# Kernel tuning notes

Hardware: AMD Instinct MI355X
Metric: run time of the kernel (lower is better)

Reference implementation:

```python
import jax, jax.numpy as jnp
import numpy as np

N_NODES = 20000
N_EDGES = 640000
D = 128            # node feature dim
NUM_HEADS = 4      # = num_irreps of edge_sh (lmax=3, 0e+1o+2e+3o)
HEAD_DIM = D // NUM_HEADS
IR_DIMS = np.array([1, 3, 5, 7])  # dims of each irrep; sum = 16
AVG_NUM_NEIGHBORS = 32.0


def setup_inputs() -> dict:
    key = jax.random.key(0)
    ks = jax.random.split(key, 20)
    inp = {
        "edge_sh": jax.random.normal(ks[0], (N_EDGES, int(IR_DIMS.sum())), jnp.float32),
        "node_feats": jax.random.normal(ks[1], (N_NODES, D), jnp.float32),
        "edge_feats": jax.random.normal(ks[2], (N_EDGES, 64), jnp.float32),
        "chi_scalar": jax.random.normal(ks[3], (N_EDGES, 64), jnp.float32),
        "cutoffs": jax.random.uniform(ks[4], (N_EDGES,), jnp.float32),
        "senders": jax.random.randint(ks[5], (N_EDGES,), 0, N_NODES),
        "receivers": jax.random.randint(ks[6], (N_EDGES,), 0, N_NODES),
        # radial MLP: 64 -> 128 -> 128 (silu between)
        "W_rad1": jax.random.normal(ks[7], (64, 128), jnp.float32) / np.sqrt(64),
        "b_rad1": jnp.zeros((128,), jnp.float32),
        "W_rad2": jax.random.normal(ks[8], (128, 128), jnp.float32) / np.sqrt(128),
        "b_rad2": jnp.zeros((128,), jnp.float32),
        # spherical-scalar MLP: 64 -> 128 -> 128
        "W_sph1": jax.random.normal(ks[9], (64, 128), jnp.float32) / np.sqrt(64),
        "b_sph1": jnp.zeros((128,), jnp.float32),
        "W_sph2": jax.random.normal(ks[10], (128, 128), jnp.float32) / np.sqrt(128),
        "b_sph2": jnp.zeros((128,), jnp.float32),
        # Q/K projections, no bias
        "Wq": jax.random.normal(ks[11], (D, D), jnp.float32) / np.sqrt(D),
        "Wk": jax.random.normal(ks[12], (D, D), jnp.float32) / np.sqrt(D),
    }
    return inp


def reference(edge_sh, node_feats, edge_feats, chi_scalar, cutoffs, senders,
              receivers, W_rad1, b_rad1, W_rad2, b_rad2, W_sph1, b_sph1,
              W_sph2, b_sph2, Wq, Wk):
    silu = jax.nn.silu
    # edge filter: radial MLP + spherical-scalar MLP
    w = silu(edge_feats @ W_rad1 + b_rad1) @ W_rad2 + b_rad2      # [E, D]
    w = w + (silu(chi_scalar @ W_sph1 + b_sph1) @ W_sph2 + b_sph2)
    w = w.reshape(-1, NUM_HEADS, HEAD_DIM)                        # [E, H, hd]
    # gathered queries/keys
    q = (node_feats @ Wq).reshape(-1, NUM_HEADS, HEAD_DIM)[receivers]
    k = (node_feats @ Wk).reshape(-1, NUM_HEADS, HEAD_DIM)[senders]
    # filter-scaled attention: per-edge, per-head scalar
    alpha = (q * w * k).sum(axis=-1) * (1.0 / np.sqrt(HEAD_DIM))  # [E, H]
    alpha = alpha * cutoffs[:, None]
    # aligned_mul: broadcast per-irrep weight over each irrep's dim (mul=1)
    y = jnp.repeat(alpha, IR_DIMS, axis=-1)                       # [E, 16]
    msg = edge_sh * y
    # scatter_sum into receivers
    chi = jax.ops.segment_sum(msg, receivers, num_segments=N_NODES)
    return chi / AVG_NUM_NEIGHBORS
```

## Files before the change

### kernel.cpp

```cpp
#include <hip/hip_runtime.h>
#include <cmath>

#define NNODES 20000
#define NEDGES 640000
#define DDIM   128
#define TN     16
#define BE     64

typedef __attribute__((ext_vector_type(8))) short bf16x8;
typedef __attribute__((ext_vector_type(4))) float f32x4;
typedef __attribute__((ext_vector_type(4))) unsigned short us4;

__device__ __forceinline__ unsigned short f2bf(float x) {
    union { float f; unsigned u; } v; v.f = x;
    unsigned r = v.u + 0x7FFFu + ((v.u >> 16) & 1u);
    return (unsigned short)(r >> 16);
}
__device__ __forceinline__ float bf2f(unsigned short h) {
    union { unsigned u; float f; } v; v.u = ((unsigned)h) << 16; return v.f;
}
__device__ __forceinline__ unsigned cvtpk(float lo, float hi) {
    unsigned r;
    asm("v_cvt_pk_bf16_f32 %0, %1, %2" : "=v"(r) : "v"(lo), "v"(hi));
    return r;
}

__global__ void pack_weights(const float* __restrict__ W, unsigned short* __restrict__ dst)
{
    const int f  = blockIdx.x;
    const int kt = f >> 3, nt = f & 7;
    const int t  = threadIdx.x;
#pragma unroll
    for (int ii = 0; ii < 2; ii++) {
        const int idx  = t * 2 + ii;
        const int lane = idx >> 3, i = idx & 7;
        const int k = kt * 32 + (lane >> 4) * 8 + i;
        const int n = nt * 16 + (lane & 15);
        dst[f * 512 + idx] = f2bf(W[k * 128 + n]);
    }
}

__global__ __launch_bounds__(256) void qk_proj_kernel(
    const float* __restrict__ nf, const float* __restrict__ Wq,
    const float* __restrict__ Wk, unsigned short* __restrict__ qbuf,
    unsigned short* __restrict__ kbuf)
{
    __shared__ float s_nf[TN * DDIM];
    const int t  = threadIdx.x;
    const int n0 = blockIdx.x * TN;
    {
        const float4* src = (const float4*)(nf + (size_t)n0 * DDIM);
        float4* dst = (float4*)s_nf;
        for (int i = t; i < TN * DDIM / 4; i += 256) dst[i] = src[i];
    }
    __syncthreads();

    const int j = t & 127;
    const float* W = (t < 128) ? Wq : Wk;
    float acc[TN];
#pragma unroll
    for (int n = 0; n < TN; n++) acc[n] = 0.f;

    for (int k = 0; k < DDIM; k += 4) {
        const float w0 = W[(k + 0) * DDIM + j];
        const float w1 = W[(k + 1) * DDIM + j];
        const float w2 = W[(k + 2) * DDIM + j];
        const float w3 = W[(k + 3) * DDIM + j];
#pragma unroll
        for (int n = 0; n < TN; n++) {
            const float4 f = *(const float4*)&s_nf[n * DDIM + k];
            acc[n] = fmaf(f.w, w3, fmaf(f.z, w2, fmaf(f.y, w1, fmaf(f.x, w0, acc[n]))));
        }
    }
    unsigned short* outp = (t < 128) ? qbuf : kbuf;
    for (int n = 0; n < TN; n++) outp[(size_t)(n0 + n) * DDIM + j] = f2bf(acc[n]);
}

__global__ __launch_bounds__(256, 4) void edge_kernel(
    const float* __restrict__ edge_sh, const float* __restrict__ cutoffs,
    const int* __restrict__ senders, const int* __restrict__ receivers,
    const float* __restrict__ edge_feats, const float* __restrict__ chi_scalar,
    const unsigned short* __restrict__ w1r, const unsigned short* __restrict__ w1s,
    const unsigned short* __restrict__ w2r, const unsigned short* __restrict__ w2s,
    const float* __restrict__ b_rad1, const float* __restrict__ b_sph1,
    const float* __restrict__ b_rad2, const float* __restrict__ b_sph2,
    const unsigned short* __restrict__ qbuf, const unsigned short* __restrict__ kbuf,
    float* __restrict__ out)
{
    __shared__ unsigned short s_a[64 * 64];
    __shared__ unsigned short s_h[64 * 128];
    __shared__ unsigned short s_p[64 * 128];
    char* pa = (char*)s_a;
    char* ph = (char*)s_h;
    char* pp = (char*)s_p;
    float* s_alpha = (float*)s_a;

    const int t  = threadIdx.x;
    const int w  = t >> 6;
    const int l  = t & 63;
    const int el = l & 15;
    const int rg = l >> 4;
    const int eb = blockIdx.x * BE;

#pragma unroll
    for (int ii = 0; ii < 8; ii++) {
        const int e  = w * 16 + ii * 2 + (l >> 5);
        const int eg = eb + e;
        const int r  = receivers[eg];
        const int s  = senders[eg];
        const int c4 = l & 31;
        const us4 qv = *(const us4*)(qbuf + (size_t)r * 128 + c4 * 4);
        const us4 kv = *(const us4*)(kbuf + (size_t)s * 128 + c4 * 4);
        const float p0 = bf2f(qv[0]) * bf2f(kv[0]);
        const float p1 = bf2f(qv[1]) * bf2f(kv[1]);
        const float p2 = bf2f(qv[2]) * bf2f(kv[2]);
        const float p3 = bf2f(qv[3]) * bf2f(kv[3]);
        const uint2 pv = { cvtpk(p0, p1), cvtpk(p2, p3) };
        *(uint2*)(pp + ((e * 256 + c4 * 8) ^ ((e & 7) << 4))) = pv;
    }

#pragma unroll
    for (int ii = 0; ii < 4; ii++) {
        const int idx = t + ii * 256;
        const int r   = idx >> 4;
        const int c4  = idx & 15;
        const float4 a = *(const float4*)(edge_feats + (size_t)(eb + r) * 64 + c4 * 4);
        const uint2 av = { cvtpk(a.x, a.y), cvtpk(a.z, a.w) };
        *(uint2*)(pa + ((r * 128 + c4 * 8) ^ ((r & 7) << 4))) = av;
    }
    __syncthreads();

    f32x4 acc2[2][4];
#pragma unroll
    for (int ct = 0; ct < 2; ct++)
#pragma unroll
        for (int et = 0; et < 4; et++)
            acc2[ct][et] = (f32x4){0.f, 0.f, 0.f, 0.f};

    {
        f32x4 acc1[2][4];
#pragma unroll
        for (int ht = 0; ht < 2; ht++)
#pragma unroll
            for (int et = 0; et < 4; et++)
                acc1[ht][et] = (f32x4){0.f, 0.f, 0.f, 0.f};

#pragma unroll
        for (int kt = 0; kt < 2; kt++) {
            bf16x8 bfrag[4];
#pragma unroll
            for (int et = 0; et < 4; et++) {
                const int e = et * 16 + el;
                const int k = kt * 32 + rg * 8;
                bfrag[et] = *(const bf16x8*)(pa + ((e * 128 + k * 2) ^ ((e & 7) << 4)));
            }
#pragma unroll
            for (int ht = 0; ht < 2; ht++) {
                const int f = kt * 8 + (w * 2 + ht);
                const bf16x8 afrag = *(const bf16x8*)(w1r + (size_t)f * 512 + l * 8);
#pragma unroll
                for (int et = 0; et < 4; et++)
                    acc1[ht][et] = __builtin_amdgcn_mfma_f32_16x16x32_bf16(
                        afrag, bfrag[et], acc1[ht][et], 0, 0, 0);
            }
        }

#pragma unroll
        for (int ht = 0; ht < 2; ht++) {
            const int hid0 = w * 32 + ht * 16 + rg * 4;
            const float4 bv = *(const float4*)(b_rad1 + hid0);
            const float* bvf = (const float*)&bv;
#pragma unroll
            for (int et = 0; et < 4; et++) {
                const int e = et * 16 + el;
                float s[4];
#pragma unroll
                for (int r = 0; r < 4; r++) {
                    const float v = acc1[ht][et][r] + bvf[r];
                    s[r] = v * __builtin_amdgcn_rcpf(1.0f + __expf(-v));
                }
                const uint2 hv = { cvtpk(s[0], s[1]), cvtpk(s[2], s[3]) };
                *(uint2*)(ph + ((e * 256 + hid0 * 2) ^ ((e & 7) << 4))) = hv;
            }
        }
        __syncthreads();

        float4 chv[4];
#pragma unroll
        for (int ii = 0; ii < 4; ii++) {
            const int idx = t + ii * 256;
            const int r   = idx >> 4;
            const int c4  = idx & 15;
            chv[ii] = *(const float4*)(chi_scalar + (size_t)(eb + r) * 64 + c4 * 4);
        }

#pragma unroll
        for (int kt = 0; kt < 4; kt++) {
            bf16x8 hfrag[4];
#pragma unroll
            for (int et = 0; et < 4; et++) {
                const int e = et * 16 + el;
                const int k = kt * 32 + rg * 8;
                hfrag[et] = *(const bf16x8*)(ph + ((e * 256 + k * 2) ^ ((e & 7) << 4)));
            }
#pragma unroll
            for (int ct = 0; ct < 2; ct++) {
                const int f = kt * 8 + (w * 2 + ct);
                const bf16x8 afrag = *(const bf16x8*)(w2r + (size_t)f * 512 + l * 8);
#pragma unroll
                for (int et = 0; et < 4; et++)
                    acc2[ct][et] = __builtin_amdgcn_mfma_f32_16x16x32_bf16(
                        afrag, hfrag[et], acc2[ct][et], 0, 0, 0);
            }
        }

#pragma unroll
        for (int ii = 0; ii < 4; ii++) {
            const int idx = t + ii * 256;
            const int r   = idx >> 4;
            const int c4  = idx & 15;
            const uint2 bv = { cvtpk(chv[ii].x, chv[ii].y), cvtpk(chv[ii].z, chv[ii].w) };
            *(uint2*)(pa + ((r * 128 + c4 * 8) ^ ((r & 7) << 4))) = bv;
        }
        __syncthreads();
    }

    {
        f32x4 acc1[2][4];
#pragma unroll
        for (int ht = 0; ht < 2; ht++)
#pragma unroll
            for (int et = 0; et < 4; et++)
                acc1[ht][et] = (f32x4){0.f, 0.f, 0.f, 0.f};

#pragma unroll
        for (int kt = 0; kt < 2; kt++) {
            bf16x8 bfrag[4];
#pragma unroll
            for (int et = 0; et < 4; et++) {
                const int e = et * 16 + el;
                const int k = kt * 32 + rg * 8;
                bfrag[et] = *(const bf16x8*)(pa + ((e * 128 + k * 2) ^ ((e & 7) << 4)));
            }
#pragma unroll
            for (int ht = 0; ht < 2; ht++) {
                const int f = kt * 8 + (w * 2 + ht);
                const bf16x8 afrag = *(const bf16x8*)(w1s + (size_t)f * 512 + l * 8);
#pragma unroll
                for (int et = 0; et < 4; et++)
                    acc1[ht][et] = __builtin_amdgcn_mfma_f32_16x16x32_bf16(
                        afrag, bfrag[et], acc1[ht][et], 0, 0, 0);
            }
        }

#pragma unroll
        for (int ht = 0; ht < 2; ht++) {
            const int hid0 = w * 32 + ht * 16 + rg * 4;
            const float4 bv = *(const float4*)(b_sph1 + hid0);
            const float* bvf = (const float*)&bv;
#pragma unroll
            for (int et = 0; et < 4; et++) {
                const int e = et * 16 + el;
                float s[4];
#pragma unroll
                for (int r = 0; r < 4; r++) {
                    const float v = acc1[ht][et][r] + bvf[r];
                    s[r] = v * __builtin_amdgcn_rcpf(1.0f + __expf(-v));
                }
                const uint2 hv = { cvtpk(s[0], s[1]), cvtpk(s[2], s[3]) };
                *(uint2*)(ph + ((e * 256 + hid0 * 2) ^ ((e & 7) << 4))) = hv;
            }
        }
        __syncthreads();

#pragma unroll
        for (int kt = 0; kt < 4; kt++) {
            bf16x8 hfrag[4];
#pragma unroll
            for (int et = 0; et < 4; et++) {
                const int e = et * 16 + el;
                const int k = kt * 32 + rg * 8;
                hfrag[et] = *(const bf16x8*)(ph + ((e * 256 + k * 2) ^ ((e & 7) << 4)));
            }
#pragma unroll
            for (int ct = 0; ct < 2; ct++) {
                const int f = kt * 8 + (w * 2 + ct);
                const bf16x8 afrag = *(const bf16x8*)(w2s + (size_t)f * 512 + l * 8);
#pragma unroll
                for (int et = 0; et < 4; et++)
                    acc2[ct][et] = __builtin_amdgcn_mfma_f32_16x16x32_bf16(
                        afrag, hfrag[et], acc2[ct][et], 0, 0, 0);
            }
        }
    }

    {
        const int c0base = w * 32 + rg * 4;
        f32x4 b2s[2];
#pragma unroll
        for (int ct = 0; ct < 2; ct++) {
            const float4 br = *(const float4*)(b_rad2 + c0base + ct * 16);
            const float4 bs = *(const float4*)(b_sph2 + c0base + ct * 16);
            b2s[ct] = (f32x4){ br.x + bs.x, br.y + bs.y, br.z + bs.z, br.w + bs.w };
        }
#pragma unroll
        for (int et = 0; et < 4; et++) {
            const int e = et * 16 + el;
            float vsum = 0.f;
#pragma unroll
            for (int ct = 0; ct < 2; ct++) {
                const int c0 = c0base + ct * 16;
                const us4 pv = *(const us4*)(pp + ((e * 256 + c0 * 2) ^ ((e & 7) << 4)));
#pragma unroll
                for (int r = 0; r < 4; r++)
                    vsum = fmaf(bf2f(pv[r]), acc2[ct][et][r] + b2s[ct][r], vsum);
            }
            vsum += __shfl_xor(vsum, 16, 64);
            vsum += __shfl_xor(vsum, 32, 64);
            if (l < 16) {
                s_alpha[(et * 16 + l) * 4 + w] = vsum * cutoffs[eb + et * 16 + l]
                                               * 0.005524271728019903f;
            }
        }
    }
    __syncthreads();

    {
        const int e   = t >> 2;
        const int c0q = t & 3;
        const int eg  = eb + e;
        const int rv  = receivers[eg];
        const float4 sh = *(const float4*)(edge_sh + (size_t)eg * 16 + c0q * 4);
        const float* shf = (const float*)&sh;
#pragma unroll
        for (int j = 0; j < 4; j++) {
            const int comp = c0q * 4 + j;
            const int head = (comp == 0) ? 0 : (comp < 4) ? 1 : (comp < 9) ? 2 : 3;
            atomicAdd(&out[(size_t)rv * 16 + comp], shf[j] * s_alpha[e * 4 + head]);
        }
    }
}

extern "C" void kernel_launch(void* const* d_in, const int* in_sizes, int n_in,
                              void* d_out, int out_size, void* d_ws, size_t ws_size,
                              hipStream_t stream)
{
    const float* edge_sh    = (const float*)d_in[0];
    const float* node_feats = (const float*)d_in[1];
    const float* edge_feats = (const float*)d_in[2];
    const float* chi_scalar = (const float*)d_in[3];
    const float* cutoffs    = (const float*)d_in[4];
    const int*   senders    = (const int*)d_in[5];
    const int*   receivers  = (const int*)d_in[6];
    const float* W_rad1 = (const float*)d_in[7];
    const float* b_rad1 = (const float*)d_in[8];
    const float* W_rad2 = (const float*)d_in[9];
    const float* b_rad2 = (const float*)d_in[10];
    const float* W_sph1 = (const float*)d_in[11];
    const float* b_sph1 = (const float*)d_in[12];
    const float* W_sph2 = (const float*)d_in[13];
    const float* b_sph2 = (const float*)d_in[14];
    const float* Wq     = (const float*)d_in[15];
    const float* Wk     = (const float*)d_in[16];

    float* out = (float*)d_out;
    unsigned short* qbuf = (unsigned short*)d_ws;
    unsigned short* kbuf = qbuf + (size_t)NNODES * DDIM;
    unsigned short* w1r  = kbuf + (size_t)NNODES * DDIM;
    unsigned short* w1s  = w1r + 16 * 512;
    unsigned short* w2r  = w1s + 16 * 512;
    unsigned short* w2s  = w2r + 32 * 512;

    hipMemsetAsync(out, 0, (size_t)out_size * sizeof(float), stream);

    pack_weights<<<16, 256, 0, stream>>>(W_rad1, w1r);
    pack_weights<<<16, 256, 0, stream>>>(W_sph1, w1s);
    pack_weights<<<32, 256, 0, stream>>>(W_rad2, w2r);
    pack_weights<<<32, 256, 0, stream>>>(W_sph2, w2s);

    qk_proj_kernel<<<NNODES / TN, 256, 0, stream>>>(node_feats, Wq, Wk, qbuf, kbuf);

    edge_kernel<<<NEDGES / BE, 256, 0, stream>>>(
        edge_sh, cutoffs, senders, receivers, edge_feats, chi_scalar,
        w1r, w1s, w2r, w2s, b_rad1, b_sph1, b_rad2, b_sph2,
        qbuf, kbuf, out);
}
```

Measured before the change: 323.1 us.

## Split q*k gather into separate kernel writing per-edge products to workspace

Moves the random gather of q[receivers]*k[senders] out of the MLP edge kernel into a dedicated p_gather kernel that writes a bf16 per-edge product buffer (about 164 MB) to the workspace. The main kernel then reads that buffer coalesced in its epilogue, drops the s_p LDS buffer, and loads edge_feats and chi_scalar into LDS together up front, which removes one barrier. The aim is to keep gather latency out of the MFMA kernel and to raise occupancy through lower LDS use. The cost is an extra round trip through HBM for the product buffer, and the path only runs when the workspace is large enough; otherwise a fallback kernel is used.

```diff
diff --git a/kernel.cpp b/kernel.cpp
--- a/kernel.cpp
+++ b/kernel.cpp
@@ -10,6 +10,7 @@
 typedef __attribute__((ext_vector_type(8))) short bf16x8;
 typedef __attribute__((ext_vector_type(4))) float f32x4;
 typedef __attribute__((ext_vector_type(4))) unsigned short us4;
+typedef __attribute__((ext_vector_type(8))) unsigned short us8;
 
 __device__ __forceinline__ unsigned short f2bf(float x) {
     union { float f; unsigned u; } v; v.f = x;
@@ -76,7 +77,200 @@
     for (int n = 0; n < TN; n++) outp[(size_t)(n0 + n) * DDIM + j] = f2bf(acc[n]);
 }
 
-__global__ __launch_bounds__(256, 4) void edge_kernel(
+__global__ __launch_bounds__(256) void p_gather(
+    const int* __restrict__ recv, const int* __restrict__ send,
+    const unsigned short* __restrict__ qbuf, const unsigned short* __restrict__ kbuf,
+    unsigned short* __restrict__ pedge)
+{
+    const int gid = blockIdx.x * 256 + threadIdx.x;
+    const int e = gid >> 4;
+    const int j = gid & 15;
+    const int r = recv[e];
+    const int s = send[e];
+    const us8 qv = *(const us8*)(qbuf + (size_t)r * 128 + j * 8);
+    const us8 kv = *(const us8*)(kbuf + (size_t)s * 128 + j * 8);
+    uint4 pv;
+    pv.x = cvtpk(bf2f(qv[0]) * bf2f(kv[0]), bf2f(qv[1]) * bf2f(kv[1]));
+    pv.y = cvtpk(bf2f(qv[2]) * bf2f(kv[2]), bf2f(qv[3]) * bf2f(kv[3]));
+    pv.z = cvtpk(bf2f(qv[4]) * bf2f(kv[4]), bf2f(qv[5]) * bf2f(kv[5]));
+    pv.w = cvtpk(bf2f(qv[6]) * bf2f(kv[6]), bf2f(qv[7]) * bf2f(kv[7]));
+    *(uint4*)(pedge + (size_t)e * 128 + j * 8) = pv;
+}
+
+__global__ __launch_bounds__(256, 4) void edge_kernel_v2(
+    const float* __restrict__ edge_sh, const float* __restrict__ cutoffs,
+    const int* __restrict__ receivers,
+    const float* __restrict__ edge_feats, const float* __restrict__ chi_scalar,
+    const unsigned short* __restrict__ w1r, const unsigned short* __restrict__ w1s,
+    const unsigned short* __restrict__ w2r, const unsigned short* __restrict__ w2s,
+    const float* __restrict__ b_rad1, const float* __restrict__ b_sph1,
+    const float* __restrict__ b_rad2, const float* __restrict__ b_sph2,
+    const unsigned short* __restrict__ pedge,
+    float* __restrict__ out)
+{
+    __shared__ unsigned short s_a[2 * 64 * 64];
+    __shared__ unsigned short s_h[64 * 128];
+    __shared__ float s_alpha[64][4];
+    char* pa = (char*)s_a;
+    char* ph = (char*)s_h;
+
+    const int t  = threadIdx.x;
+    const int w  = t >> 6;
+    const int l  = t & 63;
+    const int el = l & 15;
+    const int rg = l >> 4;
+    const int eb = blockIdx.x * BE;
+
+#pragma unroll
+    for (int ii = 0; ii < 4; ii++) {
+        const int idx = t + ii * 256;
+        const int r   = idx >> 4;
+        const int c4  = idx & 15;
+        const float4 a = *(const float4*)(edge_feats + (size_t)(eb + r) * 64 + c4 * 4);
+        const float4 b = *(const float4*)(chi_scalar + (size_t)(eb + r) * 64 + c4 * 4);
+        const uint2 av = { cvtpk(a.x, a.y), cvtpk(a.z, a.w) };
+        const uint2 bv = { cvtpk(b.x, b.y), cvtpk(b.z, b.w) };
+        const int off = (r * 128 + c4 * 8) ^ ((r & 7) << 4);
+        *(uint2*)(pa + off)        = av;
+        *(uint2*)(pa + 8192 + off) = bv;
+    }
+    __syncthreads();
+
+    f32x4 acc2[2][4];
+#pragma unroll
+    for (int ct = 0; ct < 2; ct++)
+#pragma unroll
+        for (int et = 0; et < 4; et++)
+            acc2[ct][et] = (f32x4){0.f, 0.f, 0.f, 0.f};
+
+#pragma unroll
+    for (int path = 0; path < 2; path++) {
+        const unsigned short* W1p = path ? w1s : w1r;
+        const unsigned short* W2p = path ? w2s : w2r;
+        const float* b1p = path ? b_sph1 : b_rad1;
+        const char*  ab  = pa + path * 8192;
+
+        f32x4 acc1[2][4];
+#pragma unroll
+        for (int ht = 0; ht < 2; ht++)
+#pragma unroll
+            for (int et = 0; et < 4; et++)
+                acc1[ht][et] = (f32x4){0.f, 0.f, 0.f, 0.f};
+
+#pragma unroll
+        for (int kt = 0; kt < 2; kt++) {
+            bf16x8 bfrag[4];
+#pragma unroll
+            for (int et = 0; et < 4; et++) {
+                const int e = et * 16 + el;
+                const int k = kt * 32 + rg * 8;
+                bfrag[et] = *(const bf16x8*)(ab + ((e * 128 + k * 2) ^ ((e & 7) << 4)));
+            }
+#pragma unroll
+            for (int ht = 0; ht < 2; ht++) {
+                const int f = kt * 8 + (w * 2 + ht);
+                const bf16x8 afrag = *(const bf16x8*)(W1p + (size_t)f * 512 + l * 8);
+#pragma unroll
+                for (int et = 0; et < 4; et++)
+                    acc1[ht][et] = __builtin_amdgcn_mfma_f32_16x16x32_bf16(
+                        afrag, bfrag[et], acc1[ht][et], 0, 0, 0);
+            }
+        }
+
+#pragma unroll
+        for (int ht = 0; ht < 2; ht++) {
+            const int hid0 = w * 32 + ht * 16 + rg * 4;
+            const float4 bv = *(const float4*)(b1p + hid0);
+            const float* bvf = (const float*)&bv;
+#pragma unroll
+            for (int et = 0; et < 4; et++) {
+                const int e = et * 16 + el;
+                float s[4];
+#pragma unroll
+                for (int r = 0; r < 4; r++) {
+                    const float v = acc1[ht][et][r] + bvf[r];
+                    s[r] = v * __builtin_amdgcn_rcpf(1.0f + __expf(-v));
+                }
+                const uint2 hv = { cvtpk(s[0], s[1]), cvtpk(s[2], s[3]) };
+                *(uint2*)(ph + ((e * 256 + hid0 * 2) ^ ((e & 7) << 4))) = hv;
+            }
+        }
+        __syncthreads();
+
+#pragma unroll
+        for (int kt = 0; kt < 4; kt++) {
+            bf16x8 hfrag[4];
+#pragma unroll
+            for (int et = 0; et < 4; et++) {
+                const int e = et * 16 + el;
+                const int k = kt * 32 + rg * 8;
+                hfrag[et] = *(const bf16x8*)(ph + ((e * 256 + k * 2) ^ ((e & 7) << 4)));
+            }
+#pragma unroll
+            for (int ct = 0; ct < 2; ct++) {
+                const int f = kt * 8 + (w * 2 + ct);
+                const bf16x8 afrag = *(const bf16x8*)(W2p + (size_t)f * 512 + l * 8);
+#pragma unroll
+                for (int et = 0; et < 4; et++)
+                    acc2[ct][et] = __builtin_amdgcn_mfma_f32_16x16x32_bf16(
+                        afrag, hfrag[et], acc2[ct][et], 0, 0, 0);
+            }
+        }
+        if (path == 0) __syncthreads();
+    }
+
+    {
+        const int c0base = w * 32 + rg * 4;
+        f32x4 b2s[2];
+#pragma unroll
+        for (int ct = 0; ct < 2; ct++) {
+            const float4 br = *(const float4*)(b_rad2 + c0base + ct * 16);
+            const float4 bs = *(const float4*)(b_sph2 + c0base + ct * 16);
+            b2s[ct] = (f32x4){ br.x + bs.x, br.y + bs.y, br.z + bs.z, br.w + bs.w };
+        }
+        us4 pv[2][4];
+#pragma unroll
+        for (int et = 0; et < 4; et++)
+#pragma unroll
+            for (int ct = 0; ct < 2; ct++)
+                pv[ct][et] = *(const us4*)(pedge + (size_t)(eb + et * 16 + el) * 128
+                                           + c0base + ct * 16);
+#pragma unroll
+        for (int et = 0; et < 4; et++) {
+            float vsum = 0.f;
+#pragma unroll
+            for (int ct = 0; ct < 2; ct++) {
+#pragma unroll
+                for (int r = 0; r < 4; r++)
+                    vsum = fmaf(bf2f(pv[ct][et][r]), acc2[ct][et][r] + b2s[ct][r], vsum);
+            }
+            vsum += __shfl_xor(vsum, 16, 64);
+            vsum += __shfl_xor(vsum, 32, 64);
+            if (l < 16) {
+                s_alpha[et * 16 + l][w] = vsum * cutoffs[eb + et * 16 + l]
+                                        * 0.005524271728019903f;
+            }
+        }
+    }
+    __syncthreads();
+
+    {
+        const int e   = t >> 2;
+        const int c0q = t & 3;
+        const int eg  = eb + e;
+        const int rv  = receivers[eg];
+        const float4 sh = *(const float4*)(edge_sh + (size_t)eg * 16 + c0q * 4);
+        const float* shf = (const float*)&sh;
+#pragma unroll
+        for (int j = 0; j < 4; j++) {
+            const int comp = c0q * 4 + j;
+            const int head = (comp == 0) ? 0 : (comp < 4) ? 1 : (comp < 9) ? 2 : 3;
+            atomicAdd(&out[(size_t)rv * 16 + comp], shf[j] * s_alpha[e][head]);
+        }
+    }
+}
+
+__global__ __launch_bounds__(256) void edge_kernel_fb(
     const float* __restrict__ edge_sh, const float* __restrict__ cutoffs,
     const int* __restrict__ senders, const int* __restrict__ receivers,
     const float* __restrict__ edge_feats, const float* __restrict__ chi_scalar,
@@ -87,19 +281,17 @@
     const unsigned short* __restrict__ qbuf, const unsigned short* __restrict__ kbuf,
     float* __restrict__ out)
 {
-    __shared__ unsigned short s_a[64 * 64];
+    __shared__ unsigned short s_a[2 * 64 * 64];
     __shared__ unsigned short s_h[64 * 128];
     __shared__ unsigned short s_p[64 * 128];
+    __shared__ float s_alpha[64][4];
     char* pa = (char*)s_a;
     char* ph = (char*)s_h;
     char* pp = (char*)s_p;
-    float* s_alpha = (float*)s_a;
 
     const int t  = threadIdx.x;
     const int w  = t >> 6;
     const int l  = t & 63;
-    const int el = l & 15;
-    const int rg = l >> 4;
     const int eb = blockIdx.x * BE;
 
 #pragma unroll
@@ -111,22 +303,22 @@
         const int c4 = l & 31;
         const us4 qv = *(const us4*)(qbuf + (size_t)r * 128 + c4 * 4);
         const us4 kv = *(const us4*)(kbuf + (size_t)s * 128 + c4 * 4);
-        const float p0 = bf2f(qv[0]) * bf2f(kv[0]);
-        const float p1 = bf2f(qv[1]) * bf2f(kv[1]);
-        const float p2 = bf2f(qv[2]) * bf2f(kv[2]);
-        const float p3 = bf2f(qv[3]) * bf2f(kv[3]);
-        const uint2 pv = { cvtpk(p0, p1), cvtpk(p2, p3) };
+        const uint2 pv = { cvtpk(bf2f(qv[0]) * bf2f(kv[0]), bf2f(qv[1]) * bf2f(kv[1])),
+                           cvtpk(bf2f(qv[2]) * bf2f(kv[2]), bf2f(qv[3]) * bf2f(kv[3])) };
         *(uint2*)(pp + ((e * 256 + c4 * 8) ^ ((e & 7) << 4))) = pv;
     }
-
 #pragma unroll
     for (int ii = 0; ii < 4; ii++) {
         const int idx = t + ii * 256;
         const int r   = idx >> 4;
         const int c4  = idx & 15;
         const float4 a = *(const float4*)(edge_feats + (size_t)(eb + r) * 64 + c4 * 4);
+        const float4 b = *(const float4*)(chi_scalar + (size_t)(eb + r) * 64 + c4 * 4);
         const uint2 av = { cvtpk(a.x, a.y), cvtpk(a.z, a.w) };
-        *(uint2*)(pa + ((r * 128 + c4 * 8) ^ ((r & 7) << 4))) = av;
+        const uint2 bv = { cvtpk(b.x, b.y), cvtpk(b.z, b.w) };
+        const int off = (r * 128 + c4 * 8) ^ ((r & 7) << 4);
+        *(uint2*)(pa + off)        = av;
+        *(uint2*)(pa + 8192 + off) = bv;
     }
     __syncthreads();
 
@@ -137,7 +329,13 @@
         for (int et = 0; et < 4; et++)
             acc2[ct][et] = (f32x4){0.f, 0.f, 0.f, 0.f};
 
-    {
+#pragma unroll
+    for (int path = 0; path < 2; path++) {
+        const unsigned short* W1p = path ? w1s : w1r;
+        const unsigned short* W2p = path ? w2s : w2r;
+        const float* b1p = path ? b_sph1 : b_rad1;
+        const char*  ab  = pa + path * 8192;
+
         f32x4 acc1[2][4];
 #pragma unroll
         for (int ht = 0; ht < 2; ht++)
@@ -150,29 +348,28 @@
             bf16x8 bfrag[4];
 #pragma unroll
             for (int et = 0; et < 4; et++) {
-                const int e = et * 16 + el;
-                const int k = kt * 32 + rg * 8;
-                bfrag[et] = *(const bf16x8*)(pa + ((e * 128 + k * 2) ^ ((e & 7) << 4)));
+                const int e = et * 16 + (l & 15);
+                const int k = kt * 32 + (l >> 4) * 8;
+                bfrag[et] = *(const bf16x8*)(ab + ((e * 128 + k * 2) ^ ((e & 7) << 4)));
             }
 #pragma unroll
             for (int ht = 0; ht < 2; ht++) {
                 const int f = kt * 8 + (w * 2 + ht);
-                const bf16x8 afrag = *(const bf16x8*)(w1r + (size_t)f * 512 + l * 8);
+                const bf16x8 afrag = *(const bf16x8*)(W1p + (size_t)f * 512 + l * 8);
 #pragma unroll
                 for (int et = 0; et < 4; et++)
                     acc1[ht][et] = __builtin_amdgcn_mfma_f32_16x16x32_bf16(
                         afrag, bfrag[et], acc1[ht][et], 0, 0, 0);
             }
         }
-
 #pragma unroll
         for (int ht = 0; ht < 2; ht++) {
-            const int hid0 = w * 32 + ht * 16 + rg * 4;
-            const float4 bv = *(const float4*)(b_rad1 + hid0);
+            const int hid0 = w * 32 + ht * 16 + (l >> 4) * 4;
+            const float4 bv = *(const float4*)(b1p + hid0);
             const float* bvf = (const float*)&bv;
 #pragma unroll
             for (int et = 0; et < 4; et++) {
-                const int e = et * 16 + el;
+                const int e = et * 16 + (l & 15);
                 float s[4];
 #pragma unroll
                 for (int r = 0; r < 4; r++) {
@@ -185,131 +382,44 @@
         }
         __syncthreads();
 
-        float4 chv[4];
-#pragma unroll
-        for (int ii = 0; ii < 4; ii++) {
-            const int idx = t + ii * 256;
-            const int r   = idx >> 4;
-            const int c4  = idx & 15;
-            chv[ii] = *(const float4*)(chi_scalar + (size_t)(eb + r) * 64 + c4 * 4);
-        }
-
 #pragma unroll
         for (int kt = 0; kt < 4; kt++) {
             bf16x8 hfrag[4];
 #pragma unroll
             for (int et = 0; et < 4; et++) {
-                const int e = et * 16 + el;
-                const int k = kt * 32 + rg * 8;
+                const int e = et * 16 + (l & 15);
+                const int k = kt * 32 + (l >> 4) * 8;
                 hfrag[et] = *(const bf16x8*)(ph + ((e * 256 + k * 2) ^ ((e & 7) << 4)));
             }
 #pragma unroll
             for (int ct = 0; ct < 2; ct++) {
                 const int f = kt * 8 + (w * 2 + ct);
-                const bf16x8 afrag = *(const bf16x8*)(w2r + (size_t)f * 512 + l * 8);
+                const bf16x8 afrag = *(const bf16x8*)(W2p + (size_t)f * 512 + l * 8);
 #pragma unroll
                 for (int et = 0; et < 4; et++)
                     acc2[ct][et] = __builtin_amdgcn_mfma_f32_16x16x32_bf16(
                         afrag, hfrag[et], acc2[ct][et], 0, 0, 0);
             }
         }
-
-#pragma unroll
-        for (int ii = 0; ii < 4; ii++) {
-            const int idx = t + ii * 256;
-            const int r   = idx >> 4;
-            const int c4  = idx & 15;
-            const uint2 bv = { cvtpk(chv[ii].x, chv[ii].y), cvtpk(chv[ii].z, chv[ii].w) };
-            *(uint2*)(pa + ((r * 128 + c4 * 8) ^ ((r & 7) << 4))) = bv;
-        }
-        __syncthreads();
+        if (path == 0) __syncthreads();
     }
 
     {
-        f32x4 acc1[2][4];
-#pragma unroll
-        for (int ht = 0; ht < 2; ht++)
-#pragma unroll
-            for (int et = 0; et < 4; et++)
-                acc1[ht][et] = (f32x4){0.f, 0.f, 0.f, 0.f};
-
-#pragma unroll
-        for (int kt = 0; kt < 2; kt++) {
-            bf16x8 bfrag[4];
-#pragma unroll
-            for (int et = 0; et < 4; et++) {
-                const int e = et * 16 + el;
-                const int k = kt * 32 + rg * 8;
-                bfrag[et] = *(const bf16x8*)(pa + ((e * 128 + k * 2) ^ ((e & 7) << 4)));
-            }
-#pragma unroll
-            for (int ht = 0; ht < 2; ht++) {
-                const int f = kt * 8 + (w * 2 + ht);
-                const bf16x8 afrag = *(const bf16x8*)(w1s + (size_t)f * 512 + l * 8);
-#pragma unroll
-                for (int et = 0; et < 4; et++)
-                    acc1[ht][et] = __builtin_amdgcn_mfma_f32_16x16x32_bf16(
-                        afrag, bfrag[et], acc1[ht][et], 0, 0, 0);
-            }
-        }
-
-#pragma unroll
-        for (int ht = 0; ht < 2; ht++) {
-            const int hid0 = w * 32 + ht * 16 + rg * 4;
-            const float4 bv = *(const float4*)(b_sph1 + hid0);
-            const float* bvf = (const float*)&bv;
-#pragma unroll
-            for (int et = 0; et < 4; et++) {
-                const int e = et * 16 + el;
-                float s[4];
-#pragma unroll
-                for (int r = 0; r < 4; r++) {
-                    const float v = acc1[ht][et][r] + bvf[r];
-                    s[r] = v * __builtin_amdgcn_rcpf(1.0f + __expf(-v));
-                }
-                const uint2 hv = { cvtpk(s[0], s[1]), cvtpk(s[2], s[3]) };
-                *(uint2*)(ph + ((e * 256 + hid0 * 2) ^ ((e & 7) << 4))) = hv;
-            }
-        }
-        __syncthreads();
-
-#pragma unroll
-        for (int kt = 0; kt < 4; kt++) {
-            bf16x8 hfrag[4];
-#pragma unroll
-            for (int et = 0; et < 4; et++) {
-                const int e = et * 16 + el;
-                const int k = kt * 32 + rg * 8;
-                hfrag[et] = *(const bf16x8*)(ph + ((e * 256 + k * 2) ^ ((e & 7) << 4)));
-            }
+        f32x4 b2s[2];
+#pragma unroll
+        for (int ct = 0; ct < 2; ct++) {
+            const int c0 = w * 32 + ct * 16 + (l >> 4) * 4;
+            const float4 br = *(const float4*)(b_rad2 + c0);
+            const float4 bs = *(const float4*)(b_sph2 + c0);
+            b2s[ct] = (f32x4){ br.x + bs.x, br.y + bs.y, br.z + bs.z, br.w + bs.w };
+        }
+#pragma unroll
+        for (int et = 0; et < 4; et++) {
+            const int e = et * 16 + (l & 15);
+            float vsum = 0.f;
 #pragma unroll
             for (int ct = 0; ct < 2; ct++) {
-                const int f = kt * 8 + (w * 2 + ct);
-                const bf16x8 afrag = *(const bf16x8*)(w2s + (size_t)f * 512 + l * 8);
-#pragma unroll
-                for (int et = 0; et < 4; et++)
-                    acc2[ct][et] = __builtin_amdgcn_mfma_f32_16x16x32_bf16(
-                        afrag, hfrag[et], acc2[ct][et], 0, 0, 0);
-            }
-        }
-    }
-
-    {
-        const int c0base = w * 32 + rg * 4;
-        f32x4 b2s[2];
-#pragma unroll
-        for (int ct = 0; ct < 2; ct++) {
-            const float4 br = *(const float4*)(b_rad2 + c0base + ct * 16);
-            const float4 bs = *(const float4*)(b_sph2 + c0base + ct * 16);
-            b2s[ct] = (f32x4){ br.x + bs.x, br.y + bs.y, br.z + bs.z, br.w + bs.w };
-        }
-#pragma unroll
-        for (int et = 0; et < 4; et++) {
-            const int e = et * 16 + el;
-            float vsum = 0.f;
-#pragma unroll
-            for (int ct = 0; ct < 2; ct++) {
-                const int c0 = c0base + ct * 16;
+                const int c0 = w * 32 + ct * 16 + (l >> 4) * 4;
                 const us4 pv = *(const us4*)(pp + ((e * 256 + c0 * 2) ^ ((e & 7) << 4)));
 #pragma unroll
                 for (int r = 0; r < 4; r++)
@@ -318,8 +428,8 @@
             vsum += __shfl_xor(vsum, 16, 64);
             vsum += __shfl_xor(vsum, 32, 64);
             if (l < 16) {
-                s_alpha[(et * 16 + l) * 4 + w] = vsum * cutoffs[eb + et * 16 + l]
-                                               * 0.005524271728019903f;
+                s_alpha[et * 16 + l][w] = vsum * cutoffs[eb + et * 16 + l]
+                                        * 0.005524271728019903f;
             }
         }
     }
@@ -329,14 +439,14 @@
         const int e   = t >> 2;
         const int c0q = t & 3;
         const int eg  = eb + e;
-        const int rv  = receivers[eg];
+        const int rn  = receivers[eg];
         const float4 sh = *(const float4*)(edge_sh + (size_t)eg * 16 + c0q * 4);
         const float* shf = (const float*)&sh;
 #pragma unroll
         for (int j = 0; j < 4; j++) {
             const int comp = c0q * 4 + j;
             const int head = (comp == 0) ? 0 : (comp < 4) ? 1 : (comp < 9) ? 2 : 3;
-            atomicAdd(&out[(size_t)rv * 16 + comp], shf[j] * s_alpha[e * 4 + head]);
+            atomicAdd(&out[(size_t)rn * 16 + comp], shf[j] * s_alpha[e][head]);
         }
     }
 }
@@ -370,6 +480,11 @@
     unsigned short* w1s  = w1r + 16 * 512;
     unsigned short* w2r  = w1s + 16 * 512;
     unsigned short* w2s  = w2r + 32 * 512;
+    unsigned short* pedge = w2s + 32 * 512;
+
+    const size_t need = ((size_t)((char*)pedge - (char*)d_ws))
+                      + (size_t)NEDGES * DDIM * sizeof(unsigned short);
+    const bool big = (ws_size >= need);
 
     hipMemsetAsync(out, 0, (size_t)out_size * sizeof(float), stream);
 
@@ -380,8 +495,16 @@
 
     qk_proj_kernel<<<NNODES / TN, 256, 0, stream>>>(node_feats, Wq, Wk, qbuf, kbuf);
 
-    edge_kernel<<<NEDGES / BE, 256, 0, stream>>>(
-        edge_sh, cutoffs, senders, receivers, edge_feats, chi_scalar,
-        w1r, w1s, w2r, w2s, b_rad1, b_sph1, b_rad2, b_sph2,
-        qbuf, kbuf, out);
-}
+    if (big) {
+        p_gather<<<NEDGES * 16 / 256, 256, 0, stream>>>(receivers, senders, qbuf, kbuf, pedge);
+        edge_kernel_v2<<<NEDGES / BE, 256, 0, stream>>>(
+            edge_sh, cutoffs, receivers, edge_feats, chi_scalar,
+            w1r, w1s, w2r, w2s, b_rad1, b_sph1, b_rad2, b_sph2,
+            pedge, out);
+    } else {
+        edge_kernel_fb<<<NEDGES / BE, 256, 0, stream>>>(
+            edge_sh, cutoffs, senders, receivers, edge_feats, chi_scalar,
+            w1r, w1s, w2r, w2s, b_rad1, b_sph1, b_rad2, b_sph2,
+            qbuf, kbuf, out);
+    }
+}
```

Result: slower. 353.2 us (+9.3%).
